# Performance work log

Hardware: AMD Instinct MI355X
Metric: run time of the kernel (lower is better)

The kernel has to match this reference:

```python
import jax, jax.numpy as jnp
import numpy as np

HIDDEN = 2048
N_HEAD = 16
N_KV_HEAD = 4
HEAD_DIM = HIDDEN // N_HEAD
B, S = 2, 2048


def setup_inputs() -> dict:
    key = jax.random.key(0)
    ks = jax.random.split(key, 10)
    scale = 1.0 / np.sqrt(HIDDEN)
    x = jax.random.normal(ks[0], (B, S, HIDDEN), dtype=jnp.float32)
    # causal additive mask, broadcastable over batch and heads
    causal = jnp.tril(jnp.ones((S, S), dtype=jnp.bool_))
    attention_mask = jnp.where(causal, 0.0, -1e9).astype(jnp.float32)[None, None]
    wq_w = jax.random.uniform(ks[1], (HIDDEN, HIDDEN), jnp.float32, -scale, scale)
    wq_b = jax.random.uniform(ks[2], (HIDDEN,), jnp.float32, -scale, scale)
    wk_w = jax.random.uniform(ks[3], (N_KV_HEAD * HEAD_DIM, HIDDEN), jnp.float32, -scale, scale)
    wk_b = jax.random.uniform(ks[4], (N_KV_HEAD * HEAD_DIM,), jnp.float32, -scale, scale)
    wv_w = jax.random.uniform(ks[5], (N_KV_HEAD * HEAD_DIM, HIDDEN), jnp.float32, -scale, scale)
    wv_b = jax.random.uniform(ks[6], (N_KV_HEAD * HEAD_DIM,), jnp.float32, -scale, scale)
    wo_w = jax.random.uniform(ks[7], (HIDDEN, HIDDEN), jnp.float32, -scale, scale)
    wo_b = jax.random.uniform(ks[8], (HIDDEN,), jnp.float32, -scale, scale)
    return dict(x=x, attention_mask=attention_mask, wq_w=wq_w, wq_b=wq_b,
                wk_w=wk_w, wk_b=wk_b, wv_w=wv_w, wv_b=wv_b, wo_w=wo_w, wo_b=wo_b)


def reference(x, attention_mask, wq_w, wq_b, wk_w, wk_b, wv_w, wv_b, wo_w, wo_b):
    bs, seq_len, _ = x.shape
    group = N_HEAD // N_KV_HEAD
    q = x @ wq_w.T + wq_b  # [B,S,H*D]
    k = x @ wk_w.T + wk_b  # [B,S,Hkv*D]
    v = x @ wv_w.T + wv_b
    q = q.reshape(bs, seq_len, N_HEAD, HEAD_DIM).transpose(0, 2, 1, 3)        # [B,H,S,D]
    k = k.reshape(bs, seq_len, N_KV_HEAD, HEAD_DIM).transpose(0, 2, 1, 3)     # [B,Hkv,S,D]
    v = v.reshape(bs, seq_len, N_KV_HEAD, HEAD_DIM).transpose(0, 2, 1, 3)
    # GQA: share each kv head across `group` query heads (repeat_interleave equiv)
    qg = q.reshape(bs, N_KV_HEAD, group, seq_len, HEAD_DIM)
    scores = jnp.einsum('bkgqd,bkld->bkgql', qg, k) / np.sqrt(HEAD_DIM)       # [B,Hkv,g,S,S]
    scores = scores + attention_mask[:, :, None]  # mask broadcast over head dims
    attn = jax.nn.softmax(scores, axis=-1)  # dropout is identity at inference
    out = jnp.einsum('bkgql,bkld->bkgqd', attn, v)                             # [B,Hkv,g,S,D]
    out = out.reshape(bs, N_HEAD, seq_len, HEAD_DIM).transpose(0, 2, 1, 3)
    out = out.reshape(bs, seq_len, HIDDEN)
    return out @ wo_w.T + wo_b
```

## Files before the change

### kernel.cpp

```cpp
#include <hip/hip_runtime.h>

typedef __bf16 bf16;
typedef __bf16 bf16x8 __attribute__((ext_vector_type(8)));
typedef __bf16 bf16x4 __attribute__((ext_vector_type(4)));
typedef __bf16 bf16x2 __attribute__((ext_vector_type(2)));
typedef float  f32x4  __attribute__((ext_vector_type(4)));

#define HIDDEN 2048
#define NH 16
#define NKV 4
#define HD 128
#define BB 2
#define SS 2048
#define MTOT (BB*SS)
#define KVD (NKV*HD)

__device__ __forceinline__ void gload_lds16(const void* g, void* l) {
  __builtin_amdgcn_global_load_lds(
      (__attribute__((address_space(1))) void*)(void*)g,
      (__attribute__((address_space(3))) void*)l,
      16, 0, 0);
}

__device__ __forceinline__ void pipe_barrier() {
  __builtin_amdgcn_sched_barrier(0);
  __builtin_amdgcn_s_barrier();
  __builtin_amdgcn_sched_barrier(0);
}

__global__ void detect_dtype(const unsigned short* __restrict__ x, int* __restrict__ flag) {
  __shared__ int cnt;
  if (threadIdx.x == 0) cnt = 0;
  __syncthreads();
  int c = 0;
  for (int i = threadIdx.x; i < 8192; i += blockDim.x) {
    float v = fabsf(__uint_as_float((unsigned)x[i] << 16));
    if (v > 64.0f || (v > 0.0f && v < 9.5367431640625e-07f)) ++c;
  }
  atomicAdd(&cnt, c);
  __syncthreads();
  if (threadIdx.x == 0) flag[0] = (cnt > 1024) ? 1 : 0;
}

struct ConvJobs {
  const void* src[8];
  bf16*       dst[8];
  long long   n[8];
};

__device__ __forceinline__ void conv8(const void* src, bf16* dst, long long n,
                                      int f, long long i0, long long stride) {
  const long long n8 = n >> 3;
  if (f) {
    const float4* s4 = (const float4*)src;
    for (long long i = i0; i < n8; i += stride) {
      float4 a = s4[2*i], b = s4[2*i+1];
      bf16x8 o;
      o[0]=(bf16)a.x; o[1]=(bf16)a.y; o[2]=(bf16)a.z; o[3]=(bf16)a.w;
      o[4]=(bf16)b.x; o[5]=(bf16)b.y; o[6]=(bf16)b.z; o[7]=(bf16)b.w;
      *(bf16x8*)&dst[i*8] = o;
    }
  } else {
    const bf16x8* s8 = (const bf16x8*)src;
    for (long long i = i0; i < n8; i += stride)
      *(bf16x8*)&dst[i*8] = s8[i];
  }
}

__global__ void conv_multi(ConvJobs jobs, const int* __restrict__ flag) {
  const int f = flag[0];
  const int a = blockIdx.y;
  conv8(jobs.src[a], jobs.dst[a], jobs.n[a], f,
        (long long)blockIdx.x * blockDim.x + threadIdx.x,
        (long long)gridDim.x * blockDim.x);
}

__global__ void conv_one(const void* __restrict__ src, bf16* __restrict__ dst,
                         long long n, const int* __restrict__ flag) {
  conv8(src, dst, n, flag[0],
        (long long)blockIdx.x * blockDim.x + threadIdx.x,
        (long long)gridDim.x * blockDim.x);
}

__global__ __launch_bounds__(512)
void gemm_qkv256(const bf16* __restrict__ A,
                 const bf16* __restrict__ wq, const bf16* __restrict__ bq,
                 const bf16* __restrict__ wk, const bf16* __restrict__ bk,
                 const bf16* __restrict__ wv, const bf16* __restrict__ bv,
                 bf16* __restrict__ Cq, bf16* __restrict__ Ck, bf16* __restrict__ Cvt)
{
  __shared__ bf16 Asl[2][256*32];
  __shared__ bf16 Bsl[2][256*32];
  const int bx = blockIdx.x;
  const bf16 *Wp, *bias;
  int n0, mode;
  if (bx < 8)       { Wp = wq; bias = bq; n0 = bx*256;      mode = 0; }
  else if (bx < 10) { Wp = wk; bias = bk; n0 = (bx-8)*256;  mode = 1; }
  else              { Wp = wv; bias = bv; n0 = (bx-10)*256; mode = 2; }

  const int tid  = threadIdx.x;
  const int wave = tid >> 6, lane = tid & 63;
  const int g = lane >> 4, l15 = lane & 15;
  const int wr = wave >> 2, wc = wave & 3;
  const int m0 = blockIdx.y * 256;

  f32x4 acc[8][4] = {};

  auto stage4 = [&](int nb, int k0) {
    #pragma unroll
    for (int i = 0; i < 2; ++i) {
      const int cl  = tid + i*512;
      const int row = cl >> 2, ch = cl & 3;
      const int sc  = ch ^ ((row >> 2) & 3);
      gload_lds16(A  + (size_t)(m0 + row)*HIDDEN + k0 + sc*8, &Asl[nb][cl*8]);
      gload_lds16(Wp + (size_t)(n0 + row)*HIDDEN + k0 + sc*8, &Bsl[nb][cl*8]);
    }
  };

  stage4(0, 0);
  asm volatile("s_waitcnt vmcnt(0)" ::: "memory");
  pipe_barrier();

  const int nt = HIDDEN / 32;
  int buf = 0;
  for (int t = 0; t < nt; ++t) {
    bf16x8 af[4], bfr[4];
    #pragma unroll
    for (int mi = 0; mi < 4; ++mi) {
      const int rl = wr*128 + mi*16 + l15;
      const int ch = g ^ ((rl >> 2) & 3);
      af[mi] = *(const bf16x8*)&Asl[buf][rl*32 + ch*8];
    }
    #pragma unroll
    for (int ni = 0; ni < 4; ++ni) {
      const int rl = wc*64 + ni*16 + l15;
      const int ch = g ^ ((rl >> 2) & 3);
      bfr[ni] = *(const bf16x8*)&Bsl[buf][rl*32 + ch*8];
    }
    if (t + 1 < nt) stage4(buf ^ 1, (t + 1) * 32);
    pipe_barrier();
    __builtin_amdgcn_s_setprio(1);
    #pragma unroll
    for (int mi = 0; mi < 4; ++mi)
      #pragma unroll
      for (int ni = 0; ni < 4; ++ni)
        acc[mi][ni] = __builtin_amdgcn_mfma_f32_16x16x32_bf16(af[mi], bfr[ni], acc[mi][ni], 0, 0, 0);
    __builtin_amdgcn_s_setprio(0);
    #pragma unroll
    for (int mi = 0; mi < 4; ++mi) {
      const int rl = wr*128 + 64 + mi*16 + l15;
      const int ch = g ^ ((rl >> 2) & 3);
      af[mi] = *(const bf16x8*)&Asl[buf][rl*32 + ch*8];
    }
    pipe_barrier();
    __builtin_amdgcn_s_setprio(1);
    #pragma unroll
    for (int mi = 0; mi < 4; ++mi)
      #pragma unroll
      for (int ni = 0; ni < 4; ++ni)
        acc[4+mi][ni] = __builtin_amdgcn_mfma_f32_16x16x32_bf16(af[mi], bfr[ni], acc[4+mi][ni], 0, 0, 0);
    __builtin_amdgcn_s_setprio(0);
    __builtin_amdgcn_sched_barrier(0);
    asm volatile("s_waitcnt vmcnt(0)" ::: "memory");
    __builtin_amdgcn_s_barrier();
    __builtin_amdgcn_sched_barrier(0);
    buf ^= 1;
  }

  if (mode == 2) {
    #pragma unroll
    for (int ni = 0; ni < 4; ++ni) {
      const int cc = n0 + wc*64 + ni*16 + l15;
      const float bv2 = (float)bias[cc];
      #pragma unroll
      for (int mi = 0; mi < 8; ++mi) {
        const int row = m0 + wr*128 + mi*16 + g*4;
        bf16x4 o4;
        #pragma unroll
        for (int r = 0; r < 4; ++r) o4[r] = (bf16)(acc[mi][ni][r] + bv2);
        *(bf16x4*)&Cvt[(size_t)cc*MTOT + row] = o4;
      }
    }
  } else {
    bf16* Cb = (mode == 0) ? Cq : Ck;
    const int N = (mode == 0) ? HIDDEN : KVD;
    #pragma unroll
    for (int ni = 0; ni < 4; ++ni) {
      const int col = n0 + wc*64 + ni*16 + l15;
      const float bv2 = (float)bias[col];
      #pragma unroll
      for (int mi = 0; mi < 8; ++mi) {
        const int row = m0 + wr*128 + mi*16 + g*4;
        #pragma unroll
        for (int r = 0; r < 4; ++r)
          Cb[(size_t)(row + r)*N + col] = (bf16)(acc[mi][ni][r] + bv2);
      }
    }
  }
}

__global__ __launch_bounds__(256)
void gemm_bt(const bf16* __restrict__ A, const bf16* __restrict__ W,
             const bf16* __restrict__ bias, void* __restrict__ C,
             int M, int N, int K, const int* __restrict__ flagp)
{
  __shared__ bf16 As[128*32];
  __shared__ bf16 Bs[128*32];
  const int tid  = threadIdx.x;
  const int wave = tid >> 6, lane = tid & 63;
  const int g = lane >> 4, l15 = lane & 15;
  const int m0 = blockIdx.y * 128, n0 = blockIdx.x * 128;
  const int wm = (wave >> 1) * 64, wn = (wave & 1) * 64;
  const int srow = lane >> 2;
  const int scol = (lane & 3) * 8;
  f32x4 acc[4][4] = {};

  for (int k0 = 0; k0 < K; k0 += 32) {
    #pragma unroll
    for (int i = 0; i < 2; ++i) {
      const int seg = wave*2 + i;
      const int row = seg*16 + srow;
      gload_lds16(A + (size_t)(m0+row)*K + k0 + scol, &As[row*32 + scol]);
      gload_lds16(W + (size_t)(n0+row)*K + k0 + scol, &Bs[row*32 + scol]);
    }
    asm volatile("s_waitcnt vmcnt(0)" ::: "memory");
    __syncthreads();
    bf16x8 af[4], bfr[4];
    #pragma unroll
    for (int m = 0; m < 4; ++m)
      af[m] = *(const bf16x8*)&As[(wm + m*16 + l15)*32 + g*8];
    #pragma unroll
    for (int n = 0; n < 4; ++n)
      bfr[n] = *(const bf16x8*)&Bs[(wn + n*16 + l15)*32 + g*8];
    #pragma unroll
    for (int m = 0; m < 4; ++m)
      #pragma unroll
      for (int n = 0; n < 4; ++n)
        acc[m][n] = __builtin_amdgcn_mfma_f32_16x16x32_bf16(af[m], bfr[n], acc[m][n], 0, 0, 0);
    __syncthreads();
  }
  const int outf = flagp ? flagp[0] : 0;
  if (outf) {
    float* Cf = (float*)C;
    #pragma unroll
    for (int n = 0; n < 4; ++n) {
      const int col = n0 + wn + n*16 + l15;
      const float bv = (float)bias[col];
      #pragma unroll
      for (int m = 0; m < 4; ++m) {
        const int row = m0 + wm + m*16 + g*4;
        #pragma unroll
        for (int r = 0; r < 4; ++r)
          Cf[(size_t)(row + r)*N + col] = acc[m][n][r] + bv;
      }
    }
  } else {
    bf16* Cb = (bf16*)C;
    #pragma unroll
    for (int n = 0; n < 4; ++n) {
      const int col = n0 + wn + n*16 + l15;
      const float bv = (float)bias[col];
      #pragma unroll
      for (int m = 0; m < 4; ++m) {
        const int row = m0 + wm + m*16 + g*4;
        #pragma unroll
        for (int r = 0; r < 4; ++r)
          Cb[(size_t)(row + r)*N + col] = (bf16)(acc[m][n][r] + bv);
      }
    }
  }
}

#define QB 64
#define KB2 32

__global__ __launch_bounds__(256)
void attn_fwd(const bf16* __restrict__ Q, const bf16* __restrict__ K,
              const bf16* __restrict__ Vt, bf16* __restrict__ O)
{
  __shared__ bf16 Ks[2][KB2*128];
  __shared__ bf16 Vs[2][128*KB2];
  __shared__ bf16 Pl[4][16][36];
  const int tid = threadIdx.x, wave = tid >> 6, lane = tid & 63;
  const int g = lane >> 4, l15 = lane & 15;
  const int bh = blockIdx.y;
  const int b = bh >> 4, h = bh & 15, kvh = h >> 2;
  const bf16* Qh = Q + ((size_t)b*SS)*HIDDEN + h*HD;
  const bf16* Kh = K + ((size_t)b*SS)*KVD + kvh*HD;
  const bf16* Vh = Vt + ((size_t)kvh*HD)*MTOT + (size_t)b*SS;
  bf16*       Oh = O + ((size_t)b*SS)*HIDDEN + h*HD;

  const float KSC    = 0.12751879526563404f;
  const float NEGBIG = -1.0e30f;

  const int krow_st = lane >> 4;
  const int ksc     = lane & 15;
  const int vrow_in = lane >> 2;
  const int vsrc_x  = ((lane >> 2) ^ (lane >> 4)) & 3;
  const int svr     = (l15 ^ (l15 >> 2)) & 3;

  #pragma unroll 1
  for (int pass = 0; pass < 2; ++pass) {
    const int qt = pass ? (31 - (int)blockIdx.x) : (int)blockIdx.x;
    const int qrow0 = qt*QB + wave*16;
    const int qg    = qrow0 + l15;

    bf16x8 bq[4];
    #pragma unroll
    for (int c = 0; c < 4; ++c)
      bq[c] = *(const bf16x8*)(Qh + (size_t)(qrow0 + l15)*HIDDEN + c*32 + g*8);

    f32x4 od[8] = {};
    float m_run = NEGBIG, l_part = 0.f;
    const int nt = 2*qt + 2;

    auto stage = [&](int bi, int kv0) {
      #pragma unroll
      for (int i = 0; i < 2; ++i) {
        const int s = wave*2 + i;
        const int kr = s*4 + krow_st;
        const int kc = ksc ^ (kr & 7);
        gload_lds16(Kh + (size_t)(kv0 + kr)*KVD + kc*8, &Ks[bi][s*512 + lane*8]);
        const int vr = s*16 + vrow_in;
        const int vc = (lane & 3) ^ vsrc_x;
        gload_lds16(Vh + (size_t)vr*MTOT + kv0 + vc*8, &Vs[bi][s*512 + lane*8]);
      }
    };

    stage(0, 0);
    asm volatile("s_waitcnt vmcnt(0)" ::: "memory");
    __syncthreads();

    int buf = 0;
    #pragma unroll 1
    for (int t = 0; t < nt; ++t) {
      const int kv0 = t * KB2;

      if (t + 1 < nt) stage(buf ^ 1, kv0 + KB2);

      f32x4 st[2];
      #pragma unroll
      for (int nb = 0; nb < 2; ++nb) {
        f32x4 s = {};
        #pragma unroll
        for (int c = 0; c < 4; ++c) {
          const int krow = nb*16 + l15;
          const int kch  = (c*4 + g) ^ (l15 & 7);
          bf16x8 ka = *(const bf16x8*)&Ks[buf][krow*128 + kch*8];
          s = __builtin_amdgcn_mfma_f32_16x16x32_bf16(ka, bq[c], s, 0, 0, 0);
        }
        st[nb] = s;
      }

      float x[8];
      float mt = NEGBIG;
      if (t >= nt - 2) {
        #pragma unroll
        for (int nb = 0; nb < 2; ++nb)
          #pragma unroll
          for (int r = 0; r < 4; ++r) {
            const int kv = kv0 + nb*16 + g*4 + r;
            float v = (kv <= qg) ? st[nb][r] : NEGBIG;
            x[nb*4 + r] = v;
            mt = fmaxf(mt, v);
          }
      } else {
        #pragma unroll
        for (int nb = 0; nb < 2; ++nb)
          #pragma unroll
          for (int r = 0; r < 4; ++r) {
            x[nb*4 + r] = st[nb][r];
            mt = fmaxf(mt, st[nb][r]);
          }
      }
      mt = fmaxf(mt, __shfl_xor(mt, 16, 64));
      mt = fmaxf(mt, __shfl_xor(mt, 32, 64));

      if (!__all((mt - m_run) <= 62.0f)) {
        const float m_new = fmaxf(m_run, mt);
        const float corr  = __builtin_amdgcn_exp2f((m_run - m_new) * KSC);
        l_part *= corr;
        #pragma unroll
        for (int db = 0; db < 8; ++db) od[db] *= corr;
        m_run = m_new;
      }

      float psum = 0.f;
      bf16x2 pk[2][2];
      #pragma unroll
      for (int nb = 0; nb < 2; ++nb) {
        const float p0 = __builtin_amdgcn_exp2f((x[nb*4+0] - m_run) * KSC);
        const float p1 = __builtin_amdgcn_exp2f((x[nb*4+1] - m_run) * KSC);
        const float p2 = __builtin_amdgcn_exp2f((x[nb*4+2] - m_run) * KSC);
        const float p3 = __builtin_amdgcn_exp2f((x[nb*4+3] - m_run) * KSC);
        psum += p0 + p1 + p2 + p3;
        pk[nb][0] = bf16x2{(bf16)p0, (bf16)p1};
        pk[nb][1] = bf16x2{(bf16)p2, (bf16)p3};
      }
      l_part += psum;

      #pragma unroll
      for (int nb = 0; nb < 2; ++nb) {
        *(bf16x2*)&Pl[wave][l15][nb*16 + g*4 + 0] = pk[nb][0];
        *(bf16x2*)&Pl[wave][l15][nb*16 + g*4 + 2] = pk[nb][1];
      }
      asm volatile("s_waitcnt lgkmcnt(0)" ::: "memory");
      __builtin_amdgcn_sched_barrier(0);

      {
        bf16x8 pb = *(const bf16x8*)&Pl[wave][l15][g*8];
        #pragma unroll
        for (int db = 0; db < 8; ++db) {
          const int vrow = db*16 + l15;
          const int vch  = g ^ svr;
          bf16x8 va = *(const bf16x8*)&Vs[buf][vrow*KB2 + vch*8];
          od[db] = __builtin_amdgcn_mfma_f32_16x16x32_bf16(va, pb, od[db], 0, 0, 0);
        }
      }

      asm volatile("s_waitcnt vmcnt(0)" ::: "memory");
      __syncthreads();
      buf ^= 1;
    }

    float lt = l_part;
    lt += __shfl_xor(lt, 16, 64);
    lt += __shfl_xor(lt, 32, 64);
    const float inv = 1.0f / lt;
    #pragma unroll
    for (int db = 0; db < 8; ++db) {
      bf16x4 o4;
      #pragma unroll
      for (int r = 0; r < 4; ++r) o4[r] = (bf16)(od[db][r] * inv);
      *(bf16x4*)(Oh + (size_t)qg*HIDDEN + db*16 + g*4) = o4;
    }
  }
}

extern "C" void kernel_launch(void* const* d_in, const int* in_sizes, int n_in,
                              void* d_out, int out_size, void* d_ws, size_t ws_size,
                              hipStream_t stream)
{
  (void)in_sizes; (void)n_in; (void)out_size; (void)ws_size;
  const void* x    = d_in[0];
  const void* wq_w = d_in[2];
  const void* wq_b = d_in[3];
  const void* wk_w = d_in[4];
  const void* wk_b = d_in[5];
  const void* wv_w = d_in[6];
  const void* wv_b = d_in[7];
  const void* wo_w = d_in[8];
  const void* wo_b = d_in[9];

  int*  flag = (int*)d_ws;
  bf16* base = (bf16*)((char*)d_ws + 256);
  const long long NX  = (long long)MTOT*HIDDEN;
  const long long NWQ = (long long)HIDDEN*HIDDEN;
  const long long NWK = (long long)KVD*HIDDEN;
  bf16* x_ao = base;
  bf16* wqwo = x_ao + NX;
  bf16* wk_c = wqwo + NWQ;
  bf16* wv_c = wk_c + NWK;
  bf16* bq_c = wv_c + NWK;
  bf16* bk_c = bq_c + 2048;
  bf16* bv_c = bk_c + 512;
  bf16* bo_c = bv_c + 512;
  bf16* q_ws  = bo_c + 2048;
  bf16* k_ws  = q_ws + NX;
  bf16* vt_ws = k_ws + (long long)MTOT*KVD;

  detect_dtype<<<1, 256, 0, stream>>>((const unsigned short*)x, flag);

  ConvJobs jb;
  jb.src[0] = x;    jb.dst[0] = x_ao; jb.n[0] = NX;
  jb.src[1] = wq_w; jb.dst[1] = wqwo; jb.n[1] = NWQ;
  jb.src[2] = wk_w; jb.dst[2] = wk_c; jb.n[2] = NWK;
  jb.src[3] = wv_w; jb.dst[3] = wv_c; jb.n[3] = NWK;
  jb.src[4] = wq_b; jb.dst[4] = bq_c; jb.n[4] = 2048;
  jb.src[5] = wk_b; jb.dst[5] = bk_c; jb.n[5] = 512;
  jb.src[6] = wv_b; jb.dst[6] = bv_c; jb.n[6] = 512;
  jb.src[7] = wo_b; jb.dst[7] = bo_c; jb.n[7] = 2048;
  conv_multi<<<dim3(512, 8), 256, 0, stream>>>(jb, flag);

  gemm_qkv256<<<dim3(12, MTOT/256), 512, 0, stream>>>(x_ao, wqwo, bq_c, wk_c, bk_c,
                                                      wv_c, bv_c, q_ws, k_ws, vt_ws);

  conv_one<<<dim3(512), 256, 0, stream>>>(wo_w, wqwo, NWQ, flag);

  attn_fwd<<<dim3(16, BB*NH), 256, 0, stream>>>(q_ws, k_ws, vt_ws, x_ao);

  gemm_bt<<<dim3(HIDDEN/128, MTOT/128), 256, 0, stream>>>(x_ao, wqwo, bo_c, d_out, MTOT, HIDDEN, HIDDEN, flag);
}
```

Baseline: 252.2 us.

## Enlarge attention KV tile to 64 and swizzle GEMM block order

The attention kernel now processes 64 keys per iteration instead of 32. This halves the number of loop iterations, barriers and softmax rescale checks, and widens the LDS buffers, the P staging buffer and the swizzle patterns to match. Separately, both GEMM kernels remap the block index with an XCD-style swizzle so consecutive blocks land on the same chiplet, which should improve L2 reuse. In exchange the attention kernel uses more LDS and registers, which may lower occupancy, and more masked work is done on the diagonal tile.

Result: faster. 232.4 us (-7.8%).

```diff
diff --git a/kernel.cpp b/kernel.cpp
--- a/kernel.cpp
+++ b/kernel.cpp
@@ -91,7 +91,11 @@
 {
   __shared__ bf16 Asl[2][256*32];
   __shared__ bf16 Bsl[2][256*32];
-  const int bx = blockIdx.x;
+  const int bid = blockIdx.y * 12 + blockIdx.x;
+  const int swz = (bid & 7) * 24 + (bid >> 3);
+  const int bx  = swz % 12;
+  const int by  = swz / 12;
+
   const bf16 *Wp, *bias;
   int n0, mode;
   if (bx < 8)       { Wp = wq; bias = bq; n0 = bx*256;      mode = 0; }
@@ -102,7 +106,7 @@
   const int wave = tid >> 6, lane = tid & 63;
   const int g = lane >> 4, l15 = lane & 15;
   const int wr = wave >> 2, wc = wave & 3;
-  const int m0 = blockIdx.y * 256;
+  const int m0 = by * 256;
 
   f32x4 acc[8][4] = {};
 
@@ -206,10 +210,17 @@
 {
   __shared__ bf16 As[128*32];
   __shared__ bf16 Bs[128*32];
+  const int nwg = gridDim.x * gridDim.y;
+  const int bid = blockIdx.y * gridDim.x + blockIdx.x;
+  const int cpx = nwg >> 3;
+  const int swz = (bid & 7) * cpx + (bid >> 3);
+  const int bx  = swz % gridDim.x;
+  const int by  = swz / gridDim.x;
+
   const int tid  = threadIdx.x;
   const int wave = tid >> 6, lane = tid & 63;
   const int g = lane >> 4, l15 = lane & 15;
-  const int m0 = blockIdx.y * 128, n0 = blockIdx.x * 128;
+  const int m0 = by * 128, n0 = bx * 128;
   const int wm = (wave >> 1) * 64, wn = (wave & 1) * 64;
   const int srow = lane >> 2;
   const int scol = (lane & 3) * 8;
@@ -272,15 +283,15 @@
 }
 
 #define QB 64
-#define KB2 32
+#define PPAD 72
 
 __global__ __launch_bounds__(256)
 void attn_fwd(const bf16* __restrict__ Q, const bf16* __restrict__ K,
               const bf16* __restrict__ Vt, bf16* __restrict__ O)
 {
-  __shared__ bf16 Ks[2][KB2*128];
-  __shared__ bf16 Vs[2][128*KB2];
-  __shared__ bf16 Pl[4][16][36];
+  __shared__ bf16 Ks[2][64*128];
+  __shared__ bf16 Vs[2][128*64];
+  __shared__ bf16 Pl[4][16][PPAD];
   const int tid = threadIdx.x, wave = tid >> 6, lane = tid & 63;
   const int g = lane >> 4, l15 = lane & 15;
   const int bh = blockIdx.y;
@@ -293,11 +304,10 @@
   const float KSC    = 0.12751879526563404f;
   const float NEGBIG = -1.0e30f;
 
-  const int krow_st = lane >> 4;
-  const int ksc     = lane & 15;
-  const int vrow_in = lane >> 2;
-  const int vsrc_x  = ((lane >> 2) ^ (lane >> 4)) & 3;
-  const int svr     = (l15 ^ (l15 >> 2)) & 3;
+  const int krow_st = (lane >> 4);
+  const int vrow_st = (lane >> 3);
+  const int ksc     = (lane & 15);
+  const int vsc     = (lane & 7) ^ (lane >> 3);
 
   #pragma unroll 1
   for (int pass = 0; pass < 2; ++pass) {
@@ -312,51 +322,60 @@
 
     f32x4 od[8] = {};
     float m_run = NEGBIG, l_part = 0.f;
-    const int nt = 2*qt + 2;
-
-    auto stage = [&](int bi, int kv0) {
-      #pragma unroll
-      for (int i = 0; i < 2; ++i) {
-        const int s = wave*2 + i;
+    const int ntiles = qt + 1;
+
+    {
+      const int kv0 = 0;
+      #pragma unroll
+      for (int i = 0; i < 4; ++i) {
+        const int s = wave*4 + i;
         const int kr = s*4 + krow_st;
         const int kc = ksc ^ (kr & 7);
-        gload_lds16(Kh + (size_t)(kv0 + kr)*KVD + kc*8, &Ks[bi][s*512 + lane*8]);
-        const int vr = s*16 + vrow_in;
-        const int vc = (lane & 3) ^ vsrc_x;
-        gload_lds16(Vh + (size_t)vr*MTOT + kv0 + vc*8, &Vs[bi][s*512 + lane*8]);
-      }
-    };
-
-    stage(0, 0);
+        gload_lds16(Kh + (size_t)(kv0 + kr)*KVD + kc*8, &Ks[0][s*512 + lane*8]);
+        const int vr = s*8 + vrow_st;
+        gload_lds16(Vh + (size_t)vr*MTOT + kv0 + vsc*8, &Vs[0][s*512 + lane*8]);
+      }
+    }
     asm volatile("s_waitcnt vmcnt(0)" ::: "memory");
     __syncthreads();
 
     int buf = 0;
     #pragma unroll 1
-    for (int t = 0; t < nt; ++t) {
-      const int kv0 = t * KB2;
-
-      if (t + 1 < nt) stage(buf ^ 1, kv0 + KB2);
-
-      f32x4 st[2];
-      #pragma unroll
-      for (int nb = 0; nb < 2; ++nb) {
+    for (int t = 0; t < ntiles; ++t) {
+      const int kv0 = t * 64;
+
+      if (t + 1 < ntiles) {
+        const int kv1 = kv0 + 64;
+        #pragma unroll
+        for (int i = 0; i < 4; ++i) {
+          const int s = wave*4 + i;
+          const int kr = s*4 + krow_st;
+          const int kc = ksc ^ (kr & 7);
+          gload_lds16(Kh + (size_t)(kv1 + kr)*KVD + kc*8, &Ks[buf^1][s*512 + lane*8]);
+          const int vr = s*8 + vrow_st;
+          gload_lds16(Vh + (size_t)vr*MTOT + kv1 + vsc*8, &Vs[buf^1][s*512 + lane*8]);
+        }
+      }
+
+      f32x4 st[4];
+      #pragma unroll
+      for (int nb = 0; nb < 4; ++nb) {
         f32x4 s = {};
         #pragma unroll
         for (int c = 0; c < 4; ++c) {
           const int krow = nb*16 + l15;
-          const int kch  = (c*4 + g) ^ (l15 & 7);
+          const int kch  = (c*4 + g) ^ (krow & 7);
           bf16x8 ka = *(const bf16x8*)&Ks[buf][krow*128 + kch*8];
           s = __builtin_amdgcn_mfma_f32_16x16x32_bf16(ka, bq[c], s, 0, 0, 0);
         }
         st[nb] = s;
       }
 
-      float x[8];
+      float x[16];
       float mt = NEGBIG;
-      if (t >= nt - 2) {
-        #pragma unroll
-        for (int nb = 0; nb < 2; ++nb)
+      if (t == ntiles - 1) {
+        #pragma unroll
+        for (int nb = 0; nb < 4; ++nb)
           #pragma unroll
           for (int r = 0; r < 4; ++r) {
             const int kv = kv0 + nb*16 + g*4 + r;
@@ -366,7 +385,7 @@
           }
       } else {
         #pragma unroll
-        for (int nb = 0; nb < 2; ++nb)
+        for (int nb = 0; nb < 4; ++nb)
           #pragma unroll
           for (int r = 0; r < 4; ++r) {
             x[nb*4 + r] = st[nb][r];
@@ -386,9 +405,9 @@
       }
 
       float psum = 0.f;
-      bf16x2 pk[2][2];
-      #pragma unroll
-      for (int nb = 0; nb < 2; ++nb) {
+      bf16x2 pk[4][2];
+      #pragma unroll
+      for (int nb = 0; nb < 4; ++nb) {
         const float p0 = __builtin_amdgcn_exp2f((x[nb*4+0] - m_run) * KSC);
         const float p1 = __builtin_amdgcn_exp2f((x[nb*4+1] - m_run) * KSC);
         const float p2 = __builtin_amdgcn_exp2f((x[nb*4+2] - m_run) * KSC);
@@ -400,20 +419,21 @@
       l_part += psum;
 
       #pragma unroll
-      for (int nb = 0; nb < 2; ++nb) {
+      for (int nb = 0; nb < 4; ++nb) {
         *(bf16x2*)&Pl[wave][l15][nb*16 + g*4 + 0] = pk[nb][0];
         *(bf16x2*)&Pl[wave][l15][nb*16 + g*4 + 2] = pk[nb][1];
       }
       asm volatile("s_waitcnt lgkmcnt(0)" ::: "memory");
       __builtin_amdgcn_sched_barrier(0);
 
-      {
-        bf16x8 pb = *(const bf16x8*)&Pl[wave][l15][g*8];
+      #pragma unroll
+      for (int c = 0; c < 2; ++c) {
+        bf16x8 pb = *(const bf16x8*)&Pl[wave][l15][c*32 + g*8];
         #pragma unroll
         for (int db = 0; db < 8; ++db) {
           const int vrow = db*16 + l15;
-          const int vch  = g ^ svr;
-          bf16x8 va = *(const bf16x8*)&Vs[buf][vrow*KB2 + vch*8];
+          const int vch  = (c*4 + g) ^ (l15 & 7);
+          bf16x8 va = *(const bf16x8*)&Vs[buf][vrow*64 + vch*8];
           od[db] = __builtin_amdgcn_mfma_f32_16x16x32_bf16(va, pb, od[db], 0, 0, 0);
         }
       }
```
